# Performance work log

Hardware: AMD Instinct MI355X
Metric: run time of the kernel (lower is better)

Reference implementation:

```python
import jax, jax.numpy as jnp
import numpy as np

B, T, D, H, FF, TB = 4, 512, 768, 12, 3072, 64
DK = D // H
E = float(np.e)
NEG = -1e9  # stand-in for float('-inf') masked_fill; rows always have valid entries


def layer_norm(x, g, b, eps=1e-5):
    m = jnp.mean(x, axis=-1, keepdims=True)
    v = jnp.mean((x - m) ** 2, axis=-1, keepdims=True)
    return (x - m) * jax.lax.rsqrt(v + eps) * g + b


def setup_inputs() -> dict:
    key = jax.random.key(0)
    ks = jax.random.split(key, 20)
    s = 0.02
    w = lambda k, shape: jax.random.normal(k, shape, jnp.float32) * s
    return {
        "x": jax.random.normal(ks[0], (B, T, D), jnp.float32),
        "batch_temporal_mat": jax.random.uniform(ks[1], (B, T, T), jnp.float32, 0.0, 100.0),
        "padding_masks": jnp.ones((B, 1, T, T), jnp.int32),
        # attention linears (stored (in,out): y = x @ W + b, equals torch x @ W_t.T + b)
        "wq": w(ks[2], (D, D)), "bq": w(ks[3], (D,)),
        "wk": w(ks[4], (D, D)), "bk": w(ks[5], (D,)),
        "wv": w(ks[6], (D, D)), "bv": w(ks[7], (D,)),
        "wp": w(ks[8], (D, D)), "bp": w(ks[9], (D,)),
        # temporal-bias MLP: Linear(1,TB) -> leaky_relu(0.2) -> Linear(TB,1)
        "tb1_w": w(ks[10], (1, TB)), "tb1_b": w(ks[11], (TB,)),
        "tb2_w": w(ks[12], (TB, 1)), "tb2_b": w(ks[13], (1,)),
        # FFN
        "fc1_w": w(ks[14], (D, FF)), "fc1_b": w(ks[15], (FF,)),
        "fc2_w": w(ks[16], (FF, D)), "fc2_b": w(ks[17], (D,)),
        # layernorms
        "ln1_g": jnp.ones((D,), jnp.float32), "ln1_b": jnp.zeros((D,), jnp.float32),
        "ln2_g": jnp.ones((D,), jnp.float32), "ln2_b": jnp.zeros((D,), jnp.float32),
    }


def _block(x, batch_temporal_mat, padding_masks,
           wq, bq, wk, bk, wv, bv, wp, bp,
           tb1_w, tb1_b, tb2_w, tb2_b,
           fc1_w, fc1_b, fc2_w, fc2_b,
           ln1_g, ln1_b, ln2_g, ln2_b):
    # pre-LN attention sublayer
    h = layer_norm(x, ln1_g, ln1_b)
    q = (h @ wq + bq).reshape(B, T, H, DK).transpose(0, 2, 1, 3)  # (B,H,T,DK)
    k = (h @ wk + bk).reshape(B, T, H, DK).transpose(0, 2, 1, 3)
    v = (h @ wv + bv).reshape(B, T, H, DK).transpose(0, 2, 1, 3)
    scores = jnp.einsum('bhid,bhjd->bhij', q, k) * (DK ** -0.5)  # (B,H,T,T)

    # temporal bias: 1/log(e + dt), then per-(i,j) MLP with leaky_relu(0.2)
    tm = 1.0 / jnp.log(E + batch_temporal_mat)                    # (B,T,T)
    hb = jax.nn.leaky_relu(tm[..., None] @ tb1_w + tb1_b, 0.2)    # (B,T,T,TB)
    bias = (hb @ tb2_w + tb2_b)[..., 0]                           # (B,T,T)
    scores = scores + bias[:, None]

    # padding mask then causal (future) mask with CLS row 0 fully visible
    scores = jnp.where(padding_masks == 0, NEG, scores)
    causal = jnp.triu(jnp.ones((T, T), bool), 1).at[0, :].set(False)
    scores = jnp.where(causal, NEG, scores)

    p = jax.nn.softmax(scores, axis=-1)
    out = jnp.einsum('bhij,bhjd->bhid', p, v).transpose(0, 2, 1, 3).reshape(B, T, D)
    out = out @ wp + bp
    x = x + out

    # pre-LN FFN sublayer (exact GELU as in nn.GELU default)
    h2 = layer_norm(x, ln2_g, ln2_b)
    m = jax.nn.gelu(h2 @ fc1_w + fc1_b, approximate=False) @ fc2_w + fc2_b
    return x + m


def reference(x, batch_temporal_mat, padding_masks,
              wq, bq, wk, bk, wv, bv, wp, bp,
              tb1_w, tb1_b, tb2_w, tb2_b,
              fc1_w, fc1_b, fc2_w, fc2_b,
              ln1_g, ln1_b, ln2_g, ln2_b):
    return _block(x, batch_temporal_mat, padding_masks,
                  wq, bq, wk, bk, wv, bv, wp, bp,
                  tb1_w, tb1_b, tb2_w, tb2_b,
                  fc1_w, fc1_b, fc2_w, fc2_b,
                  ln1_g, ln1_b, ln2_g, ln2_b)
```

## Files before the change

kernel.cpp:

```cpp
#include <hip/hip_runtime.h>
#include <hip/hip_bf16.h>
#include <math.h>

#define B_ 4
#define T_ 512
#define D_ 768
#define H_ 12
#define FF_ 3072
#define DK_ 64
#define NTOK (B_*T_)
#define NEGV -1e9f

typedef unsigned short u16;
typedef __bf16 bfx8 __attribute__((ext_vector_type(8)));
typedef float f32x4 __attribute__((ext_vector_type(4)));
typedef u16 u16x8 __attribute__((ext_vector_type(8)));

__device__ __forceinline__ u16 f2bf(float f) {
  union { float f; unsigned u; } v; v.f = f;
  unsigned r = (v.u + 0x7FFFu + ((v.u >> 16) & 1u)) >> 16;
  return (u16)r;
}

__device__ __forceinline__ void glds16(const u16* g, u16* l) {
  __builtin_amdgcn_global_load_lds((const __attribute__((address_space(1))) void*)g,
                                   (__attribute__((address_space(3))) void*)l, 16, 0, 0);
}

__global__ __launch_bounds__(256) void prep_kernel(
    const float* __restrict__ x,
    const float* __restrict__ wq, const float* __restrict__ wk,
    const float* __restrict__ wv, const float* __restrict__ wp,
    const float* __restrict__ fc1, const float* __restrict__ fc2,
    u16* wqT, u16* wkT, u16* wvT, u16* wpT, u16* fc1T, u16* fc2T,
    const float* __restrict__ ln1g, const float* __restrict__ ln1b, u16* __restrict__ hbuf,
    const float* __restrict__ bp, float* __restrict__ x1,
    const float* __restrict__ tmat, const int* __restrict__ pad,
    const float* __restrict__ tb1w, const float* __restrict__ tb1b,
    const float* __restrict__ tb2w, const float* __restrict__ tb2b,
    float* __restrict__ biasM)
{
  const int bid = blockIdx.x;
  const int tid = threadIdx.x;
  if (bid < 6912) {
    __shared__ float tile[32][33];
    const float* in; u16* outp; int K, N, local;
    if (bid < 2304) {
      int m = bid / 576; local = bid % 576; K = 768; N = 768;
      in   = m == 0 ? wq  : (m == 1 ? wk  : (m == 2 ? wv  : wp));
      outp = m == 0 ? wqT : (m == 1 ? wkT : (m == 2 ? wvT : wpT));
    } else if (bid < 4608) {
      local = bid - 2304; K = 768; N = 3072; in = fc1; outp = fc1T;
    } else {
      local = bid - 4608; K = 3072; N = 768; in = fc2; outp = fc2T;
    }
    const int nt = N / 32;
    const int n0 = (local % nt) * 32, k0 = (local / nt) * 32;
    const int tx = tid & 31, ty = tid >> 5;
    #pragma unroll
    for (int i = 0; i < 4; ++i) {
      int r = ty + i * 8;
      tile[r][tx] = in[(size_t)(k0 + r) * N + n0 + tx];
    }
    __syncthreads();
    #pragma unroll
    for (int i = 0; i < 4; ++i) {
      int r = ty + i * 8;
      outp[(size_t)(n0 + r) * K + k0 + tx] = f2bf(tile[tx][r]);
    }
  } else if (bid < 8960) {
    const int row = bid - 6912;
    const float* xr = x + (size_t)row * D_;
    float v0 = xr[tid], v1 = xr[tid + 256], v2 = xr[tid + 512];
    float s = v0 + v1 + v2;
    float sq = v0 * v0 + v1 * v1 + v2 * v2;
    #pragma unroll
    for (int o = 32; o > 0; o >>= 1) { s += __shfl_down(s, o); sq += __shfl_down(sq, o); }
    __shared__ float ss[4], s2[4];
    int w = tid >> 6;
    if ((tid & 63) == 0) { ss[w] = s; s2[w] = sq; }
    __syncthreads();
    s = ss[0] + ss[1] + ss[2] + ss[3];
    sq = s2[0] + s2[1] + s2[2] + s2[3];
    float mean = s * (1.0f / 768.0f);
    float inv = rsqrtf(sq * (1.0f / 768.0f) - mean * mean + 1e-5f);
    u16* orow = hbuf + (size_t)row * D_;
    float* x1r = x1 + (size_t)row * D_;
    orow[tid]       = f2bf((v0 - mean) * inv * ln1g[tid]       + ln1b[tid]);
    orow[tid + 256] = f2bf((v1 - mean) * inv * ln1g[tid + 256] + ln1b[tid + 256]);
    orow[tid + 512] = f2bf((v2 - mean) * inv * ln1g[tid + 512] + ln1b[tid + 512]);
    x1r[tid]       = v0 + bp[tid];
    x1r[tid + 256] = v1 + bp[tid + 256];
    x1r[tid + 512] = v2 + bp[tid + 512];
  } else {
    __shared__ float sw1[64], sb1[64], sw2[64];
    if (tid < 64) {
      sw1[tid] = tb1w[tid];
      sb1[tid] = tb1b[tid];
      sw2[tid] = tb2w[tid];
    }
    __syncthreads();
    size_t idx = (size_t)(bid - 8960) * 256 + tid;
    float tm = 1.0f / __logf(2.718281828459045f + tmat[idx]);
    float acc = tb2b[0];
    #pragma unroll
    for (int t = 0; t < 64; ++t) {
      float u = fmaf(tm, sw1[t], sb1[t]);
      u = u > 0.0f ? u : 0.2f * u;
      acc = fmaf(u, sw2[t], acc);
    }
    biasM[idx] = (pad[idx] == 0) ? NEGV : acc;
  }
}

__device__ __forceinline__ void gemm_tile_p2(
    const u16* __restrict__ A, const u16* __restrict__ BT,
    int K, int nk, int m0, int n0, int k0,
    u16* As, u16* Bs, f32x4 acc[4][4])
{
  const int tid = threadIdx.x;
  const int w = tid >> 6, lane = tid & 63;
  const int lr = lane & 15, lk = (lane >> 4) * 8;
  const int wm = (w >> 1) * 64, wn = (w & 1) * 64;
  const int c0 = w * 64 + lane, c1 = 256 + c0;
  const int r0 = c0 >> 2, o0 = (c0 & 3) * 8;
  const int r1 = c1 >> 2, o1 = (c1 & 3) * 8;
  const u16* gA0 = A  + (size_t)(m0 + r0) * K + k0 + o0;
  const u16* gA1 = A  + (size_t)(m0 + r1) * K + k0 + o1;
  const u16* gB0 = BT + (size_t)(n0 + r0) * K + k0 + o0;
  const u16* gB1 = BT + (size_t)(n0 + r1) * K + k0 + o1;
  u16* la0 = As + w * 512;
  u16* la1 = As + 2048 + w * 512;
  u16* lb0 = Bs + w * 512;
  u16* lb1 = Bs + 2048 + w * 512;
#define ISSUE_TILE(kk, b) do { \
    glds16(gA0 + (size_t)(kk) * 32, la0 + (b) * 4096); \
    glds16(gA1 + (size_t)(kk) * 32, la1 + (b) * 4096); \
    glds16(gB0 + (size_t)(kk) * 32, lb0 + (b) * 4096); \
    glds16(gB1 + (size_t)(kk) * 32, lb1 + (b) * 4096); } while (0)
  ISSUE_TILE(0, 0);
  if (nk > 1) ISSUE_TILE(1, 1);
  int cb = 0;
  for (int kt = 0; kt < nk; ++kt) {
    if (kt < nk - 2) asm volatile("s_waitcnt vmcnt(4)" ::: "memory");
    else             asm volatile("s_waitcnt vmcnt(0)" ::: "memory");
    __builtin_amdgcn_sched_barrier(0);
    __builtin_amdgcn_s_barrier();
    __builtin_amdgcn_sched_barrier(0);
    const u16* Asc = As + cb * 4096;
    const u16* Bsc = Bs + cb * 4096;
    bfx8 af[4], bfr[4];
    #pragma unroll
    for (int t = 0; t < 4; ++t) {
      af[t]  = *(const bfx8*)&Asc[(wm + t * 16 + lr) * 32 + lk];
      bfr[t] = *(const bfx8*)&Bsc[(wn + t * 16 + lr) * 32 + lk];
    }
    #pragma unroll
    for (int rt = 0; rt < 4; ++rt)
      #pragma unroll
      for (int ct = 0; ct < 4; ++ct)
        acc[rt][ct] = __builtin_amdgcn_mfma_f32_16x16x32_bf16(af[rt], bfr[ct], acc[rt][ct], 0, 0, 0);
    if (kt + 2 < nk) {
      int nb = cb + 2; if (nb >= 3) nb -= 3;
      ISSUE_TILE(kt + 2, nb);
    }
    cb = cb + 1; if (cb >= 3) cb = 0;
  }
#undef ISSUE_TILE
}

__global__ __launch_bounds__(256) void gemm_qkv(
    const u16* __restrict__ A,
    const u16* __restrict__ wqT, const u16* __restrict__ wkT, const u16* __restrict__ wvT,
    const float* __restrict__ bq, const float* __restrict__ bk, const float* __restrict__ bv,
    u16* __restrict__ qo, u16* __restrict__ ko, u16* __restrict__ vo)
{
  __shared__ u16 As[3 * 128 * 32];
  __shared__ u16 Bs[3 * 128 * 32];
  const int z = blockIdx.z;
  const u16* BT = z == 0 ? wqT : (z == 1 ? wkT : wvT);
  const float* bias = z == 0 ? bq : (z == 1 ? bk : bv);
  u16* outp = z == 0 ? qo : (z == 1 ? ko : vo);
  const float scale = z == 0 ? 0.125f : 1.0f;
  const int m0 = blockIdx.y * 128, n0 = blockIdx.x * 128;
  f32x4 acc[4][4];
  #pragma unroll
  for (int a = 0; a < 4; ++a)
    #pragma unroll
    for (int bb = 0; bb < 4; ++bb) acc[a][bb] = (f32x4){0.f, 0.f, 0.f, 0.f};
  gemm_tile_p2(A, BT, D_, D_ / 32, m0, n0, 0, As, Bs, acc);
  const int tid = threadIdx.x;
  const int w = tid >> 6, lane = tid & 63;
  const int lr = lane & 15;
  const int wm = (w >> 1) * 64, wn = (w & 1) * 64;
  #pragma unroll
  for (int rt = 0; rt < 4; ++rt)
    #pragma unroll
    for (int ct = 0; ct < 4; ++ct)
      #pragma unroll
      for (int r = 0; r < 4; ++r) {
        int m = m0 + wm + rt * 16 + (lane >> 4) * 4 + r;
        int n = n0 + wn + ct * 16 + lr;
        float val = (acc[rt][ct][r] + bias[n]) * scale;
        int b = m >> 9, t = m & 511, hh = n >> 6, d = n & 63;
        if (z < 2) outp[(((size_t)b * H_ + hh) * T_ + t) * DK_ + d] = f2bf(val);
        else       outp[(((size_t)b * H_ + hh) * DK_ + d) * T_ + t] = f2bf(val);
      }
}

__global__ __launch_bounds__(256) void gemm_atomic(
    const u16* __restrict__ A, const u16* __restrict__ BT,
    float* __restrict__ dst, int M, int N, int K, int Ksplit)
{
  __shared__ u16 As[3 * 128 * 32];
  __shared__ u16 Bs[3 * 128 * 32];
  const int m0 = blockIdx.y * 128, n0 = blockIdx.x * 128;
  const int kz = blockIdx.z;
  f32x4 acc[4][4];
  #pragma unroll
  for (int a = 0; a < 4; ++a)
    #pragma unroll
    for (int bb = 0; bb < 4; ++bb) acc[a][bb] = (f32x4){0.f, 0.f, 0.f, 0.f};
  gemm_tile_p2(A, BT, K, Ksplit / 32, m0, n0, kz * Ksplit, As, Bs, acc);
  const int tid = threadIdx.x;
  const int w = tid >> 6, lane = tid & 63;
  const int lr = lane & 15;
  const int wm = (w >> 1) * 64, wn = (w & 1) * 64;
  #pragma unroll
  for (int rt = 0; rt < 4; ++rt)
    #pragma unroll
    for (int ct = 0; ct < 4; ++ct)
      #pragma unroll
      for (int r = 0; r < 4; ++r) {
        int m = m0 + wm + rt * 16 + (lane >> 4) * 4 + r;
        int n = n0 + wn + ct * 16 + lr;
        atomicAdd(&dst[(size_t)m * N + n], acc[rt][ct][r]);
      }
}

__global__ __launch_bounds__(256) void gemm_gelu(
    const u16* __restrict__ A, const u16* __restrict__ BT,
    const float* __restrict__ bias, u16* __restrict__ outp, int M, int N, int K)
{
  __shared__ u16 As[3 * 128 * 32];
  __shared__ u16 Bs[3 * 128 * 32];
  const int m0 = blockIdx.y * 128, n0 = blockIdx.x * 128;
  f32x4 acc[4][4];
  #pragma unroll
  for (int a = 0; a < 4; ++a)
    #pragma unroll
    for (int bb = 0; bb < 4; ++bb) acc[a][bb] = (f32x4){0.f, 0.f, 0.f, 0.f};
  gemm_tile_p2(A, BT, K, K / 32, m0, n0, 0, As, Bs, acc);
  const int tid = threadIdx.x;
  const int w = tid >> 6, lane = tid & 63;
  const int lr = lane & 15;
  const int wm = (w >> 1) * 64, wn = (w & 1) * 64;
  #pragma unroll
  for (int rt = 0; rt < 4; ++rt)
    #pragma unroll
    for (int ct = 0; ct < 4; ++ct)
      #pragma unroll
      for (int r = 0; r < 4; ++r) {
        int m = m0 + wm + rt * 16 + (lane >> 4) * 4 + r;
        int n = n0 + wn + ct * 16 + lr;
        float val = acc[rt][ct][r] + bias[n];
        float gl = 0.5f * val * (1.0f + erff(val * 0.7071067811865475f));
        outp[(size_t)m * N + n] = f2bf(gl);
      }
}

__global__ __launch_bounds__(256) void ln2_kernel(
    const float* __restrict__ x1, const float* __restrict__ g, const float* __restrict__ bta,
    const float* __restrict__ fc2b, u16* __restrict__ h2, float* __restrict__ outInit)
{
  const int row = blockIdx.x;
  const int tid = threadIdx.x;
  const size_t base = (size_t)row * D_;
  float v[3];
  float s = 0.f, sq = 0.f;
  #pragma unroll
  for (int i = 0; i < 3; ++i) {
    int c = tid + i * 256;
    float val = x1[base + c];
    v[i] = val;
    s += val; sq += val * val;
  }
  #pragma unroll
  for (int o = 32; o > 0; o >>= 1) { s += __shfl_down(s, o); sq += __shfl_down(sq, o); }
  __shared__ float ss[4], s2[4];
  int w = tid >> 6;
  if ((tid & 63) == 0) { ss[w] = s; s2[w] = sq; }
  __syncthreads();
  s = ss[0] + ss[1] + ss[2] + ss[3];
  sq = s2[0] + s2[1] + s2[2] + s2[3];
  float mean = s * (1.0f / 768.0f);
  float inv = rsqrtf(sq * (1.0f / 768.0f) - mean * mean + 1e-5f);
  #pragma unroll
  for (int i = 0; i < 3; ++i) {
    int c = tid + i * 256;
    h2[base + c] = f2bf((v[i] - mean) * inv * g[c] + bta[c]);
    outInit[base + c] = v[i] + fc2b[c];
  }
}

__global__ __launch_bounds__(256) void attn_kernel(
    const u16* __restrict__ q, const u16* __restrict__ k, const u16* __restrict__ vT,
    const float* __restrict__ biasM, u16* __restrict__ ao)
{
  __shared__ u16 P[32 * 512];
  __shared__ float pmax[128], psum[128];
  const int tid = threadIdx.x;
  const int w = tid >> 6, lane = tid & 63;
  const int lr = lane & 15, hi = lane >> 4, lk = hi * 8;

  const int bid = blockIdx.x;
  const int xcd = bid & 7, idx = bid >> 3;
  const int bh = xcd * 6 + (idx >> 4);
  const int i0 = (idx & 15) * 32;
  const int b = bh / H_, h = bh % H_;
  const int tmax = (i0 == 0) ? 31 : ((i0 >> 4) + 1);
  const int nks  = (i0 == 0) ? 16 : ((i0 >> 5) + 1);

  bfx8 qf[2][2];
  #pragma unroll
  for (int g = 0; g < 2; ++g)
    #pragma unroll
    for (int ks = 0; ks < 2; ++ks)
      qf[g][ks] = *(const bfx8*)(q + ((size_t)bh * T_ + i0 + g * 16 + lr) * DK_ + ks * 32 + lk);
  f32x4 acc[8][2];
  float mx[2][4];
  #pragma unroll
  for (int g = 0; g < 2; ++g)
    #pragma unroll
    for (int r = 0; r < 4; ++r) mx[g][r] = -3.4e38f;
  #pragma unroll
  for (int ct = 0; ct < 8; ++ct) {
    const int t = ct * 4 + w;
    if (t > tmax) continue;
    const int j0 = t * 16;
    bfx8 kf0 = *(const bfx8*)(k + ((size_t)bh * T_ + j0 + lr) * DK_ + lk);
    bfx8 kf1 = *(const bfx8*)(k + ((size_t)bh * T_ + j0 + lr) * DK_ + 32 + lk);
    const int j = j0 + lr;
    #pragma unroll
    for (int g = 0; g < 2; ++g) {
      f32x4 a0 = (f32x4){0.f, 0.f, 0.f, 0.f};
      a0 = __builtin_amdgcn_mfma_f32_16x16x32_bf16(qf[g][0], kf0, a0, 0, 0, 0);
      a0 = __builtin_amdgcn_mfma_f32_16x16x32_bf16(qf[g][1], kf1, a0, 0, 0, 0);
      #pragma unroll
      for (int r = 0; r < 4; ++r) {
        int i = i0 + g * 16 + hi * 4 + r;
        float s = a0[r] + biasM[((size_t)b * T_ + i) * T_ + j];
        if (j > i && i != 0) s = NEGV;
        a0[r] = s;
        mx[g][r] = fmaxf(mx[g][r], s);
      }
      acc[ct][g] = a0;
    }
  }
  #pragma unroll
  for (int o = 1; o < 16; o <<= 1)
    #pragma unroll
    for (int g = 0; g < 2; ++g)
      #pragma unroll
      for (int r = 0; r < 4; ++r) mx[g][r] = fmaxf(mx[g][r], __shfl_xor(mx[g][r], o));
  if (lr == 0) {
    #pragma unroll
    for (int g = 0; g < 2; ++g)
      #pragma unroll
      for (int r = 0; r < 4; ++r) pmax[w * 32 + g * 16 + hi * 4 + r] = mx[g][r];
  }
  __syncthreads();

  float M2[2][4], sm[2][4];
  #pragma unroll
  for (int g = 0; g < 2; ++g)
    #pragma unroll
    for (int r = 0; r < 4; ++r) {
      int row = g * 16 + hi * 4 + r;
      M2[g][r] = fmaxf(fmaxf(pmax[row], pmax[32 + row]), fmaxf(pmax[64 + row], pmax[96 + row]));
      sm[g][r] = 0.f;
    }
  char* Pb = (char*)P;
  #pragma unroll
  for (int ct = 0; ct < 8; ++ct) {
    const int t = ct * 4 + w;
    if (t > tmax) continue;
    const int col = t * 16 + lr;
    #pragma unroll
    for (int g = 0; g < 2; ++g)
      #pragma unroll
      for (int r = 0; r < 4; ++r) {
        float pexp = __expf(acc[ct][g][r] - M2[g][r]);
        sm[g][r] += pexp;
        int row = g * 16 + hi * 4 + r;
        int byte = (row * 1024 + col * 2) ^ ((row & 7) << 4);
        *(u16*)(Pb + byte) = f2bf(pexp);
      }
  }
  #pragma unroll
  for (int o = 1; o < 16; o <<= 1)
    #pragma unroll
    for (int g = 0; g < 2; ++g)
      #pragma unroll
      for (int r = 0; r < 4; ++r) sm[g][r] += __shfl_xor(sm[g][r], o);
  if (lr == 0) {
    #pragma unroll
    for (int g = 0; g < 2; ++g)
      #pragma unroll
      for (int r = 0; r < 4; ++r) psum[w * 32 + g * 16 + hi * 4 + r] = sm[g][r];
  }
  __syncthreads();

  float rinv[2][4];
  #pragma unroll
  for (int g = 0; g < 2; ++g)
    #pragma unroll
    for (int r = 0; r < 4; ++r) {
      int row = g * 16 + hi * 4 + r;
      rinv[g][r] = 1.0f / (psum[row] + psum[32 + row] + psum[64 + row] + psum[96 + row]);
    }

  {
    const int n0 = w * 16;
    f32x4 oa0 = (f32x4){0.f, 0.f, 0.f, 0.f};
    f32x4 oa1 = (f32x4){0.f, 0.f, 0.f, 0.f};
    for (int ks = 0; ks < nks; ++ks) {
      bfx8 vf = *(const bfx8*)(vT + ((size_t)bh * DK_ + n0 + lr) * T_ + ks * 32 + lk);
      int byte0 = (lr * 1024 + (ks * 32 + lk) * 2) ^ ((lr & 7) << 4);
      int byte1 = ((16 + lr) * 1024 + (ks * 32 + lk) * 2) ^ ((lr & 7) << 4);
      bfx8 pa0 = *(const bfx8*)(Pb + byte0);
      bfx8 pa1 = *(const bfx8*)(Pb + byte1);
      oa0 = __builtin_amdgcn_mfma_f32_16x16x32_bf16(pa0, vf, oa0, 0, 0, 0);
      oa1 = __builtin_amdgcn_mfma_f32_16x16x32_bf16(pa1, vf, oa1, 0, 0, 0);
    }
    #pragma unroll
    for (int r = 0; r < 4; ++r) {
      int i = i0 + hi * 4 + r;
      ao[((size_t)b * T_ + i) * D_ + h * DK_ + n0 + lr] = f2bf(oa0[r] * rinv[0][r]);
    }
    #pragma unroll
    for (int r = 0; r < 4; ++r) {
      int i = i0 + 16 + hi * 4 + r;
      ao[((size_t)b * T_ + i) * D_ + h * DK_ + n0 + lr] = f2bf(oa1[r] * rinv[1][r]);
    }
  }
}

extern "C" void kernel_launch(void* const* d_in, const int* in_sizes, int n_in,
                              void* d_out, int out_size, void* d_ws, size_t ws_size,
                              hipStream_t stream) {
  (void)in_sizes; (void)n_in; (void)out_size; (void)ws_size;
  const float* x    = (const float*)d_in[0];
  const float* tmat = (const float*)d_in[1];
  const int*   pad  = (const int*)d_in[2];
  const float* wq = (const float*)d_in[3];  const float* bq = (const float*)d_in[4];
  const float* wk = (const float*)d_in[5];  const float* bk = (const float*)d_in[6];
  const float* wv = (const float*)d_in[7];  const float* bv = (const float*)d_in[8];
  const float* wp = (const float*)d_in[9];  const float* bp = (const float*)d_in[10];
  const float* tb1w = (const float*)d_in[11]; const float* tb1b = (const float*)d_in[12];
  const float* tb2w = (const float*)d_in[13]; const float* tb2b = (const float*)d_in[14];
  const float* fc1w = (const float*)d_in[15]; const float* fc1b = (const float*)d_in[16];
  const float* fc2w = (const float*)d_in[17]; const float* fc2b = (const float*)d_in[18];
  const float* ln1g = (const float*)d_in[19]; const float* ln1b = (const float*)d_in[20];
  const float* ln2g = (const float*)d_in[21]; const float* ln2b = (const float*)d_in[22];
  float* out = (float*)d_out;

  char* p = (char*)d_ws;
  u16* wqT  = (u16*)p; p += (size_t)768 * 768 * 2;
  u16* wkT  = (u16*)p; p += (size_t)768 * 768 * 2;
  u16* wvT  = (u16*)p; p += (size_t)768 * 768 * 2;
  u16* wpT  = (u16*)p; p += (size_t)768 * 768 * 2;
  u16* fc1T = (u16*)p; p += (size_t)768 * 3072 * 2;
  u16* fc2T = (u16*)p; p += (size_t)3072 * 768 * 2;
  float* x1 = (float*)p; p += (size_t)NTOK * D_ * 4;
  u16* gbuf = (u16*)p; p += (size_t)NTOK * FF_ * 2;
  u16* hbuf = (u16*)p; p += (size_t)NTOK * D_ * 2;
  u16* qb   = (u16*)p; p += (size_t)NTOK * D_ * 2;
  u16* kb   = (u16*)p; p += (size_t)NTOK * D_ * 2;
  u16* vTb  = (u16*)p; p += (size_t)NTOK * D_ * 2;
  float* biasM = (float*)p; p += (size_t)B_ * T_ * T_ * 4;
  u16* ao   = (u16*)p; p += (size_t)NTOK * D_ * 2;
  u16* h2   = (u16*)p; p += (size_t)NTOK * D_ * 2;

  prep_kernel<<<13056, 256, 0, stream>>>(x, wq, wk, wv, wp, fc1w, fc2w,
                                         wqT, wkT, wvT, wpT, fc1T, fc2T,
                                         ln1g, ln1b, hbuf, bp, x1,
                                         tmat, pad, tb1w, tb1b, tb2w, tb2b, biasM);

  gemm_qkv<<<dim3(6, 16, 3), 256, 0, stream>>>(hbuf, wqT, wkT, wvT, bq, bk, bv, qb, kb, vTb);
  attn_kernel<<<768, 256, 0, stream>>>(qb, kb, vTb, biasM, ao);

  gemm_atomic<<<dim3(6, 16, 2), 256, 0, stream>>>(ao, wpT, x1, NTOK, 768, 768, 384);
  ln2_kernel<<<NTOK, 256, 0, stream>>>(x1, ln2g, ln2b, fc2b, h2, out);

  gemm_gelu<<<dim3(24, 16), 256, 0, stream>>>(h2, fc1T, fc1b, gbuf, NTOK, FF_, 768);

  gemm_atomic<<<dim3(6, 16, 4), 256, 0, stream>>>(gbuf, fc2T, out, NTOK, 768, 3072, 768);
}
```

Measured before the change: 148.5 us.

## Replace split-K atomic GEMMs with 128x64 tiles fusing bias and residual

Swaps the split-K atomicAdd GEMMs for the output projection and FC2 for a new full-K GEMM using 128x64 tiles. Bias and the residual are added in the epilogue and the result is stored directly. This removes the residual/bias pre-initialisation writes in prep and ln2 and avoids float atomics. Blocks are mapped to XCDs so neighbouring M-tiles share a die. The trade-off is fewer blocks (192), each running the full K loop, so parallelism per GEMM drops, especially for the K=3072 FC2.

```diff
diff --git a/kernel.cpp b/kernel.cpp
--- a/kernel.cpp
+++ b/kernel.cpp
@@ -34,7 +34,6 @@
     const float* __restrict__ fc1, const float* __restrict__ fc2,
     u16* wqT, u16* wkT, u16* wvT, u16* wpT, u16* fc1T, u16* fc2T,
     const float* __restrict__ ln1g, const float* __restrict__ ln1b, u16* __restrict__ hbuf,
-    const float* __restrict__ bp, float* __restrict__ x1,
     const float* __restrict__ tmat, const int* __restrict__ pad,
     const float* __restrict__ tb1w, const float* __restrict__ tb1b,
     const float* __restrict__ tb2w, const float* __restrict__ tb2b,
@@ -85,13 +84,9 @@
     float mean = s * (1.0f / 768.0f);
     float inv = rsqrtf(sq * (1.0f / 768.0f) - mean * mean + 1e-5f);
     u16* orow = hbuf + (size_t)row * D_;
-    float* x1r = x1 + (size_t)row * D_;
     orow[tid]       = f2bf((v0 - mean) * inv * ln1g[tid]       + ln1b[tid]);
     orow[tid + 256] = f2bf((v1 - mean) * inv * ln1g[tid + 256] + ln1b[tid + 256]);
     orow[tid + 512] = f2bf((v2 - mean) * inv * ln1g[tid + 512] + ln1b[tid + 512]);
-    x1r[tid]       = v0 + bp[tid];
-    x1r[tid + 256] = v1 + bp[tid + 256];
-    x1r[tid + 512] = v2 + bp[tid + 512];
   } else {
     __shared__ float sw1[64], sb1[64], sw2[64];
     if (tid < 64) {
@@ -115,7 +110,7 @@
 
 __device__ __forceinline__ void gemm_tile_p2(
     const u16* __restrict__ A, const u16* __restrict__ BT,
-    int K, int nk, int m0, int n0, int k0,
+    int K, int nk, int m0, int n0,
     u16* As, u16* Bs, f32x4 acc[4][4])
 {
   const int tid = threadIdx.x;
@@ -125,10 +120,10 @@
   const int c0 = w * 64 + lane, c1 = 256 + c0;
   const int r0 = c0 >> 2, o0 = (c0 & 3) * 8;
   const int r1 = c1 >> 2, o1 = (c1 & 3) * 8;
-  const u16* gA0 = A  + (size_t)(m0 + r0) * K + k0 + o0;
-  const u16* gA1 = A  + (size_t)(m0 + r1) * K + k0 + o1;
-  const u16* gB0 = BT + (size_t)(n0 + r0) * K + k0 + o0;
-  const u16* gB1 = BT + (size_t)(n0 + r1) * K + k0 + o1;
+  const u16* gA0 = A  + (size_t)(m0 + r0) * K + o0;
+  const u16* gA1 = A  + (size_t)(m0 + r1) * K + o1;
+  const u16* gB0 = BT + (size_t)(n0 + r0) * K + o0;
+  const u16* gB1 = BT + (size_t)(n0 + r1) * K + o1;
   u16* la0 = As + w * 512;
   u16* la1 = As + 2048 + w * 512;
   u16* lb0 = Bs + w * 512;
@@ -188,7 +183,7 @@
   for (int a = 0; a < 4; ++a)
     #pragma unroll
     for (int bb = 0; bb < 4; ++bb) acc[a][bb] = (f32x4){0.f, 0.f, 0.f, 0.f};
-  gemm_tile_p2(A, BT, D_, D_ / 32, m0, n0, 0, As, Bs, acc);
+  gemm_tile_p2(A, BT, D_, D_ / 32, m0, n0, As, Bs, acc);
   const int tid = threadIdx.x;
   const int w = tid >> 6, lane = tid & 63;
   const int lr = lane & 15;
@@ -208,33 +203,86 @@
       }
 }
 
-__global__ __launch_bounds__(256) void gemm_atomic(
+__global__ __launch_bounds__(256) void gemm_res(
     const u16* __restrict__ A, const u16* __restrict__ BT,
-    float* __restrict__ dst, int M, int N, int K, int Ksplit)
+    const float* __restrict__ bias, const float* __restrict__ resid,
+    float* __restrict__ outp, int K)
 {
   __shared__ u16 As[3 * 128 * 32];
-  __shared__ u16 Bs[3 * 128 * 32];
-  const int m0 = blockIdx.y * 128, n0 = blockIdx.x * 128;
-  const int kz = blockIdx.z;
-  f32x4 acc[4][4];
+  __shared__ u16 Bs[3 * 64 * 32];
+  const int bid = blockIdx.x;
+  const int xcd = bid & 7, i = bid >> 3;
+  const int mt = xcd * 2 + (i >= 12 ? 1 : 0);
+  const int nt = i - (i >= 12 ? 12 : 0);
+  const int m0 = mt * 128, n0 = nt * 64;
+  const int nk = K / 32;
+
+  const int tid = threadIdx.x;
+  const int w = tid >> 6, lane = tid & 63;
+  const int lr = lane & 15, hi = lane >> 4, lk = hi * 8;
+  const int wm = (w >> 1) * 64, wn = (w & 1) * 32;
+  const int c0 = w * 64 + lane, c1 = 256 + c0;
+  const int rA0 = c0 >> 2, oA0 = (c0 & 3) * 8;
+  const int rA1 = c1 >> 2, oA1 = (c1 & 3) * 8;
+  const int rB  = c0 >> 2, oB  = (c0 & 3) * 8;
+  const u16* gA0 = A  + (size_t)(m0 + rA0) * K + oA0;
+  const u16* gA1 = A  + (size_t)(m0 + rA1) * K + oA1;
+  const u16* gB  = BT + (size_t)(n0 + rB) * K + oB;
+  u16* la0 = As + w * 512;
+  u16* la1 = As + 2048 + w * 512;
+  u16* lb  = Bs + w * 512;
+
+  f32x4 acc[4][2];
   #pragma unroll
   for (int a = 0; a < 4; ++a)
     #pragma unroll
-    for (int bb = 0; bb < 4; ++bb) acc[a][bb] = (f32x4){0.f, 0.f, 0.f, 0.f};
-  gemm_tile_p2(A, BT, K, Ksplit / 32, m0, n0, kz * Ksplit, As, Bs, acc);
-  const int tid = threadIdx.x;
-  const int w = tid >> 6, lane = tid & 63;
-  const int lr = lane & 15;
-  const int wm = (w >> 1) * 64, wn = (w & 1) * 64;
+    for (int bb = 0; bb < 2; ++bb) acc[a][bb] = (f32x4){0.f, 0.f, 0.f, 0.f};
+
+#define ISSUE_T(kk, b) do { \
+    glds16(gA0 + (size_t)(kk) * 32, la0 + (b) * 4096); \
+    glds16(gA1 + (size_t)(kk) * 32, la1 + (b) * 4096); \
+    glds16(gB  + (size_t)(kk) * 32, lb  + (b) * 2048); } while (0)
+  ISSUE_T(0, 0);
+  if (nk > 1) ISSUE_T(1, 1);
+  int cb = 0;
+  for (int kt = 0; kt < nk; ++kt) {
+    if (kt < nk - 2) asm volatile("s_waitcnt vmcnt(3)" ::: "memory");
+    else             asm volatile("s_waitcnt vmcnt(0)" ::: "memory");
+    __builtin_amdgcn_sched_barrier(0);
+    __builtin_amdgcn_s_barrier();
+    __builtin_amdgcn_sched_barrier(0);
+    const u16* Asc = As + cb * 4096;
+    const u16* Bsc = Bs + cb * 2048;
+    bfx8 af[4], bfr[2];
+    #pragma unroll
+    for (int t = 0; t < 4; ++t)
+      af[t] = *(const bfx8*)&Asc[(wm + t * 16 + lr) * 32 + lk];
+    #pragma unroll
+    for (int u = 0; u < 2; ++u)
+      bfr[u] = *(const bfx8*)&Bsc[(wn + u * 16 + lr) * 32 + lk];
+    #pragma unroll
+    for (int rt = 0; rt < 4; ++rt)
+      #pragma unroll
+      for (int ct = 0; ct < 2; ++ct)
+        acc[rt][ct] = __builtin_amdgcn_mfma_f32_16x16x32_bf16(af[rt], bfr[ct], acc[rt][ct], 0, 0, 0);
+    if (kt + 2 < nk) {
+      int nb = cb + 2; if (nb >= 3) nb -= 3;
+      ISSUE_T(kt + 2, nb);
+    }
+    cb = cb + 1; if (cb >= 3) cb = 0;
+  }
+#undef ISSUE_T
+
   #pragma unroll
   for (int rt = 0; rt < 4; ++rt)
     #pragma unroll
-    for (int ct = 0; ct < 4; ++ct)
+    for (int ct = 0; ct < 2; ++ct)
       #pragma unroll
       for (int r = 0; r < 4; ++r) {
-        int m = m0 + wm + rt * 16 + (lane >> 4) * 4 + r;
+        int m = m0 + wm + rt * 16 + hi * 4 + r;
         int n = n0 + wn + ct * 16 + lr;
-        atomicAdd(&dst[(size_t)m * N + n], acc[rt][ct][r]);
+        size_t off = (size_t)m * D_ + n;
+        outp[off] = acc[rt][ct][r] + bias[n] + resid[off];
       }
 }
 
@@ -250,7 +298,7 @@
   for (int a = 0; a < 4; ++a)
     #pragma unroll
     for (int bb = 0; bb < 4; ++bb) acc[a][bb] = (f32x4){0.f, 0.f, 0.f, 0.f};
-  gemm_tile_p2(A, BT, K, K / 32, m0, n0, 0, As, Bs, acc);
+  gemm_tile_p2(A, BT, K, K / 32, m0, n0, As, Bs, acc);
   const int tid = threadIdx.x;
   const int w = tid >> 6, lane = tid & 63;
   const int lr = lane & 15;
@@ -271,7 +319,7 @@
 
 __global__ __launch_bounds__(256) void ln2_kernel(
     const float* __restrict__ x1, const float* __restrict__ g, const float* __restrict__ bta,
-    const float* __restrict__ fc2b, u16* __restrict__ h2, float* __restrict__ outInit)
+    u16* __restrict__ h2)
 {
   const int row = blockIdx.x;
   const int tid = threadIdx.x;
@@ -299,7 +347,6 @@
   for (int i = 0; i < 3; ++i) {
     int c = tid + i * 256;
     h2[base + c] = f2bf((v[i] - mean) * inv * g[c] + bta[c]);
-    outInit[base + c] = v[i] + fc2b[c];
   }
 }
 
@@ -484,16 +531,16 @@
 
   prep_kernel<<<13056, 256, 0, stream>>>(x, wq, wk, wv, wp, fc1w, fc2w,
                                          wqT, wkT, wvT, wpT, fc1T, fc2T,
-                                         ln1g, ln1b, hbuf, bp, x1,
+                                         ln1g, ln1b, hbuf,
                                          tmat, pad, tb1w, tb1b, tb2w, tb2b, biasM);
 
   gemm_qkv<<<dim3(6, 16, 3), 256, 0, stream>>>(hbuf, wqT, wkT, wvT, bq, bk, bv, qb, kb, vTb);
   attn_kernel<<<768, 256, 0, stream>>>(qb, kb, vTb, biasM, ao);
 
-  gemm_atomic<<<dim3(6, 16, 2), 256, 0, stream>>>(ao, wpT, x1, NTOK, 768, 768, 384);
-  ln2_kernel<<<NTOK, 256, 0, stream>>>(x1, ln2g, ln2b, fc2b, h2, out);
+  gemm_res<<<192, 256, 0, stream>>>(ao, wpT, bp, x, x1, 768);
+  ln2_kernel<<<NTOK, 256, 0, stream>>>(x1, ln2g, ln2b, h2);
 
   gemm_gelu<<<dim3(24, 16), 256, 0, stream>>>(h2, fc1T, fc1b, gbuf, NTOK, FF_, 768);
 
-  gemm_atomic<<<dim3(6, 16, 4), 256, 0, stream>>>(gbuf, fc2T, out, NTOK, 768, 3072, 768);
-}
+  gemm_res<<<192, 256, 0, stream>>>(gbuf, fc2T, fc2b, x1, out, 3072);
+}
```

After: 151.1 us. Within noise of the previous version (+1.7%).
